# Kernel optimization log

Measured on AMD Instinct MI355X. Metric: run time of the kernel, lower is better.

The kernel has to match this reference:

```python
import jax, jax.numpy as jnp
import numpy as np

B, S, D = 32, 512, 512
GH, LH = 8, 4            # global / local num_heads
W, STRIDE = 10, 5        # local window size and hop (window_size // 2)


def _mha(x, w_in, b_in, w_out, b_out, n_heads, key_mask=None):
    """Torch nn.MultiheadAttention (self-attn, eval mode). x: [N, L, D]."""
    N, L, d = x.shape
    dh = d // n_heads
    qkv = x @ w_in.T + b_in                       # [N, L, 3D]
    q, k, v = jnp.split(qkv, 3, axis=-1)
    def heads(t):
        return t.reshape(N, L, n_heads, dh).transpose(0, 2, 1, 3)  # [N,H,L,dh]
    q, k, v = heads(q), heads(k), heads(v)
    scores = jnp.einsum('bhqd,bhkd->bhqk', q, k) / jnp.sqrt(jnp.asarray(dh, x.dtype))
    if key_mask is not None:                      # key_mask: [N, L] bool, True = valid
        scores = jnp.where(key_mask[:, None, None, :], scores, jnp.asarray(-1e9, x.dtype))
    attn = jax.nn.softmax(scores, axis=-1)
    out = jnp.einsum('bhqk,bhkd->bhqd', attn, v).transpose(0, 2, 1, 3).reshape(N, L, d)
    return out @ w_out.T + b_out


def setup_inputs() -> dict:
    key = jax.random.key(0)
    ks = jax.random.split(key, 12)
    s = 0.02
    return {
        'x':      jax.random.normal(ks[0], (B, S, D), jnp.float32),
        'gw_in':  jax.random.normal(ks[1], (3 * D, D), jnp.float32) * s,
        'gb_in':  jnp.zeros((3 * D,), jnp.float32),
        'gw_out': jax.random.normal(ks[2], (D, D), jnp.float32) * s,
        'gb_out': jnp.zeros((D,), jnp.float32),
        'lw_in':  jax.random.normal(ks[3], (3 * D, D), jnp.float32) * s,
        'lb_in':  jnp.zeros((3 * D,), jnp.float32),
        'lw_out': jax.random.normal(ks[4], (D, D), jnp.float32) * s,
        'lb_out': jnp.zeros((D,), jnp.float32),
        'fw':     jax.random.normal(ks[5], (D, 2 * D), jnp.float32) * s,
        'fb':     jnp.zeros((D,), jnp.float32),
    }


def reference(x, gw_in, gb_in, gw_out, gb_out, lw_in, lb_in, lw_out, lb_out, fw, fb):
    # ---- global branch: full self-attention over the sequence ----
    global_out = _mha(x, gw_in, gb_in, gw_out, gb_out, GH)

    # ---- local branch: overlapping windows of size W, hop STRIDE ----
    starts = np.arange(0, S, STRIDE)              # static window starts
    NW = len(starts)
    pos = starts[:, None] + np.arange(W)          # [NW, W] absolute positions
    valid = pos < S                               # ragged tail windows
    idx = np.minimum(pos, S - 1)                  # clipped gather indices

    windows = x[:, idx]                           # [B, NW, W, D]
    windows = windows.reshape(B * NW, W, D)
    key_mask = jnp.broadcast_to(jnp.asarray(valid)[None], (B, NW, W)).reshape(B * NW, W)

    local_attn = _mha(windows, lw_in, lb_in, lw_out, lb_out, LH, key_mask=key_mask)
    local_attn = local_attn.reshape(B, NW, W, D) * jnp.asarray(valid)[None, :, :, None].astype(x.dtype)

    # scatter-add overlapping window outputs back (matches `local_out[:, i:end] +=`)
    local_out = jnp.zeros_like(x).at[:, idx.reshape(-1)].add(local_attn.reshape(B, NW * W, D))

    # ---- fusion MLP (dropout = identity in eval) ----
    combined = jnp.concatenate([global_out, local_out], axis=-1)   # [B, S, 2D]
    return jax.nn.relu(combined @ fw.T + fb)
```

## Files before the change

kernel.cpp:

```cpp
#include <hip/hip_runtime.h>
#include <cstdint>
#include <cstddef>

#define DEV __device__ __forceinline__

typedef float f32x4 __attribute__((ext_vector_type(4)));
typedef short bf16x8 __attribute__((ext_vector_type(8)));

DEV unsigned short f2bf(float f) {
  union { float f; unsigned u; } v; v.f = f;
  unsigned u = v.u;
  unsigned r = u + 0x7FFFu + ((u >> 16) & 1u);
  return (unsigned short)(r >> 16);
}
DEV unsigned short f2bf_hu(float f) {
  union { float f; unsigned u; } v; v.f = f;
  return (unsigned short)((v.u + 0x8000u) >> 16);
}
DEV float bf2f(unsigned short h) {
  union { unsigned u; float f; } v; v.u = ((unsigned)h) << 16;
  return v.f;
}

DEV void gload16(const void* g, void* l) {
  __builtin_amdgcn_global_load_lds((const __attribute__((address_space(1))) unsigned int*)g,
                                   (__attribute__((address_space(3))) unsigned int*)l,
                                   16, 0, 0);
}

DEV f32x4 MFMA(bf16x8 a, bf16x8 b, f32x4 c) {
  return __builtin_amdgcn_mfma_f32_16x16x32_bf16(a, b, c, 0, 0, 0);
}

__global__ void k_f2bf(const float* __restrict__ src, unsigned short* __restrict__ dst, int n) {
  int i = (blockIdx.x * blockDim.x + threadIdx.x) * 4;
  int stride = gridDim.x * blockDim.x * 4;
  for (; i < n; i += stride) {
    float4 v = *(const float4*)(src + i);
    ushort4 o;
    o.x = f2bf(v.x); o.y = f2bf(v.y); o.z = f2bf(v.z); o.w = f2bf(v.w);
    *(ushort4*)(dst + i) = o;
  }
}

__global__ __launch_bounds__(256) void k_merge(const float* __restrict__ fw,
                                               const float* __restrict__ gw_out,
                                               const float* __restrict__ lw_out,
                                               unsigned short* __restrict__ M1b,
                                               unsigned short* __restrict__ M2b) {
  __shared__ float Fa[64][68];
  __shared__ float Gb[64][68];
  const int bi = blockIdx.x, bj = blockIdx.y, m2 = blockIdx.z;
  const float* g = m2 ? lw_out : gw_out;
  const int i0 = bi * 64, j0 = bj * 64;
  const int tid = threadIdx.x;
  const int tr = tid >> 4, tc = tid & 15;
  float acc[4][4] = {};
  for (int kc = 0; kc < 8; kc++) {
    int k0 = kc * 64;
    __syncthreads();
    #pragma unroll
    for (int it = 0; it < 4; it++) {
      int r = tr + 16 * it;
      float4 v = *(const float4*)(fw + (size_t)(i0 + r) * 1024 + m2 * 512 + k0 + tc * 4);
      Fa[tc * 4 + 0][r] = v.x; Fa[tc * 4 + 1][r] = v.y;
      Fa[tc * 4 + 2][r] = v.z; Fa[tc * 4 + 3][r] = v.w;
      *(float4*)&Gb[r][tc * 4] = *(const float4*)(g + (size_t)(k0 + r) * 512 + j0 + tc * 4);
    }
    __syncthreads();
    for (int k = 0; k < 64; k++) {
      float4 a4 = *(const float4*)&Fa[k][tr * 4];
      float4 b4 = *(const float4*)&Gb[k][tc * 4];
      float av[4] = {a4.x, a4.y, a4.z, a4.w};
      float bv[4] = {b4.x, b4.y, b4.z, b4.w};
      #pragma unroll
      for (int r = 0; r < 4; r++)
        #pragma unroll
        for (int c = 0; c < 4; c++)
          acc[r][c] += av[r] * bv[c];
    }
  }
  unsigned short* M = m2 ? M2b : M1b;
  #pragma unroll
  for (int r = 0; r < 4; r++) {
    ushort4 pk;
    pk.x = f2bf(acc[r][0]); pk.y = f2bf(acc[r][1]);
    pk.z = f2bf(acc[r][2]); pk.w = f2bf(acc[r][3]);
    *(ushort4*)&M[(size_t)(i0 + tr * 4 + r) * 512 + j0 + tc * 4] = pk;
  }
}

__global__ __launch_bounds__(256) void k_bias(const float* __restrict__ fw, const float* __restrict__ gb_out,
                                              const float* __restrict__ lb_out, const float* __restrict__ fb,
                                              float* __restrict__ bias1, float* __restrict__ bias2) {
  __shared__ float bv[512];
  const int which = blockIdx.y;
  const int i0 = blockIdx.x * 64;
  const float* src = which ? lb_out : gb_out;
  for (int t = threadIdx.x; t < 512; t += 256) bv[t] = src[t];
  __syncthreads();
  const int r = threadIdx.x >> 2, c4 = threadIdx.x & 3;
  const float* frow = fw + (size_t)(i0 + r) * 1024 + (which ? 512 : 0) + c4 * 128;
  float a = 0.f;
  #pragma unroll 4
  for (int k = 0; k < 128; k += 4) {
    float4 v = *(const float4*)(frow + k);
    a += v.x * bv[c4 * 128 + k] + v.y * bv[c4 * 128 + k + 1]
       + v.z * bv[c4 * 128 + k + 2] + v.w * bv[c4 * 128 + k + 3];
  }
  a += __shfl_xor(a, 1);
  a += __shfl_xor(a, 2);
  if (c4 == 0) {
    int i = i0 + r;
    if (which) bias2[i] = a;
    else       bias1[i] = a + fb[i];
  }
}

template <int EPI>
__global__ __launch_bounds__(256) void k_gemm(const unsigned short* __restrict__ A,
                                              const unsigned short* __restrict__ A2,
                                              const unsigned short* __restrict__ Wm,
                                              const unsigned short* __restrict__ W2,
                                              const float* __restrict__ bias,
                                              const float* __restrict__ bias2,
                                              float qscale, void* __restrict__ Cout,
                                              int Ntot, int NT) {
  __shared__ unsigned short As[2][128 * 32];
  __shared__ unsigned short Bs[2][128 * 32];
  const int tid = threadIdx.x;
  const int wave = tid >> 6, lane = tid & 63;
  const int wr = wave >> 1, wc = wave & 1;
  const int bm = blockIdx.x, bn = blockIdx.y;
  const int ql = lane & 15, kg = lane >> 4;

  const int c0 = wave * 2;
  const int srow = lane >> 2;
  const int sks = (lane & 3) * 8;

  auto stage = [&](int buf, int t) {
    const unsigned short* sA = A;
    const unsigned short* sW = Wm;
    int k0 = t * 32;
    if (EPI == 1 && t >= 16) { sA = A2; sW = W2; k0 = (t - 16) * 32; }
    #pragma unroll
    for (int i = 0; i < 2; i++) {
      int c = c0 + i;
      int row = c * 16 + srow;
      gload16(sA + (size_t)(bm * 128 + row) * 512 + k0 + sks, &As[buf][c * 512 + lane * 8]);
      gload16(sW + (size_t)(bn * 128 + row) * 512 + k0 + sks, &Bs[buf][c * 512 + lane * 8]);
    }
  };

  f32x4 acc[4][4] = {};
  stage(0, 0);
  __syncthreads();
  for (int t = 0; t < NT; t++) {
    int buf = t & 1;
    if (t + 1 < NT) stage(buf ^ 1, t + 1);
    const unsigned short* as = As[buf];
    const unsigned short* bs = Bs[buf];
    bf16x8 af[4], bfr[4];
    #pragma unroll
    for (int m = 0; m < 4; m++)
      af[m] = *(const bf16x8*)&as[(wr * 64 + m * 16 + ql) * 32 + kg * 8];
    #pragma unroll
    for (int n = 0; n < 4; n++)
      bfr[n] = *(const bf16x8*)&bs[(wc * 64 + n * 16 + ql) * 32 + kg * 8];
    #pragma unroll
    for (int m = 0; m < 4; m++)
      #pragma unroll
      for (int n = 0; n < 4; n++)
        acc[m][n] = MFMA(af[m], bfr[n], acc[m][n]);
    __syncthreads();
  }

  const int row0 = bm * 128 + wr * 64;
  const int col0 = bn * 128 + wc * 64;
  if (EPI == 0) {
    unsigned short* C = (unsigned short*)Cout;
    #pragma unroll
    for (int m = 0; m < 4; m++)
      #pragma unroll
      for (int n = 0; n < 4; n++) {
        int col = col0 + n * 16 + ql;
        float bcol = bias[col];
        float qs = (col < 512) ? qscale : 1.0f;
        #pragma unroll
        for (int r = 0; r < 4; r++) {
          int row = row0 + m * 16 + kg * 4 + r;
          C[(size_t)row * Ntot + col] = f2bf((acc[m][n][r] + bcol) * qs);
        }
      }
  } else {
    float* C = (float*)Cout;
    #pragma unroll
    for (int m = 0; m < 4; m++)
      #pragma unroll
      for (int n = 0; n < 4; n++) {
        int col = col0 + n * 16 + ql;
        float b1 = bias[col], b2 = bias2[col];
        #pragma unroll
        for (int r = 0; r < 4; r++) {
          int row = row0 + m * 16 + kg * 4 + r;
          float cc = ((row & 511) < 5) ? 1.0f : 2.0f;
          float v = acc[m][n][r] + b1 + cc * b2;
          C[(size_t)row * 512 + col] = fmaxf(v, 0.0f);
        }
      }
  }
}

__global__ __launch_bounds__(512, 2) void k_attn_g(const unsigned short* __restrict__ QKV,
                                                   unsigned short* __restrict__ Og) {
  __shared__ unsigned short Klds[512 * 64];
  __shared__ unsigned short Vt[64][536];
  __shared__ unsigned short Plds[8][16 * 72];
  const int tid = threadIdx.x, wave = tid >> 6, lane = tid & 63;
  const int ql = lane & 15, kg = lane >> 4;
  const int h = blockIdx.x, b = blockIdx.y;
  const size_t tb = (size_t)b * 512;
  const size_t hoff = (size_t)h * 64;

  #pragma unroll
  for (int i = 0; i < 8; i++) {
    int instr = wave * 8 + i;
    int row = instr * 8 + (lane >> 3);
    int slot = lane & 7;
    int c = slot ^ (row & 7);
    gload16(QKV + (tb + row) * 1536 + 512 + hoff + c * 8, &Klds[instr * 512 + lane * 8]);
  }
  {
    const unsigned short* Vp = QKV + (tb + tid) * 1536 + 1024 + hoff;
    #pragma unroll
    for (int c8 = 0; c8 < 8; c8++) {
      bf16x8 v8 = *(const bf16x8*)(Vp + c8 * 8);
      #pragma unroll
      for (int j = 0; j < 8; j++) Vt[c8 * 8 + j][tid] = (unsigned short)v8[j];
    }
  }
  bf16x8 qf[4][2];
  #pragma unroll
  for (int m = 0; m < 4; m++) {
    const unsigned short* Qp = QKV + (tb + wave * 64 + m * 16 + ql) * 1536 + hoff;
    qf[m][0] = *(const bf16x8*)(Qp + kg * 8);
    qf[m][1] = *(const bf16x8*)(Qp + 32 + kg * 8);
  }
  __syncthreads();

  float l_part[4][4] = {};
  f32x4 o[4][4] = {};
  unsigned short* P = &Plds[wave][0];

  for (int kv = 0; kv < 8; kv++) {
    const int k0 = kv * 64;
    bf16x8 kf[4][2], vb[4][2];
    #pragma unroll
    for (int f = 0; f < 4; f++) {
      int row = k0 + 16 * f + ql;
      #pragma unroll
      for (int c = 0; c < 2; c++)
        kf[f][c] = *(const bf16x8*)&Klds[row * 64 + (((c * 4 + kg) ^ (row & 7)) * 8)];
      #pragma unroll
      for (int st = 0; st < 2; st++)
        vb[f][st] = *(const bf16x8*)&Vt[16 * f + ql][k0 + st * 32 + kg * 8];
    }
    #pragma unroll
    for (int m = 0; m < 4; m++) {
      f32x4 s[4] = {};
      #pragma unroll
      for (int f = 0; f < 4; f++) {
        s[f] = MFMA(qf[m][0], kf[f][0], s[f]);
        s[f] = MFMA(qf[m][1], kf[f][1], s[f]);
      }
      #pragma unroll
      for (int f = 0; f < 4; f++)
        #pragma unroll
        for (int r = 0; r < 4; r++)
          s[f][r] = exp2f(s[f][r]);
      #pragma unroll
      for (int r = 0; r < 4; r++)
        l_part[m][r] += (s[0][r] + s[1][r]) + (s[2][r] + s[3][r]);
      #pragma unroll
      for (int f = 0; f < 4; f++) {
        int chunk = (2 * f + (ql >> 3)) ^ kg;
        #pragma unroll
        for (int r = 0; r < 4; r++)
          P[(kg * 4 + r) * 72 + chunk * 8 + (ql & 7)] = f2bf_hu(s[f][r]);
      }
      #pragma unroll
      for (int st = 0; st < 2; st++) {
        bf16x8 pa = *(const bf16x8*)&P[ql * 72 + (((st * 4 + kg) ^ (ql >> 2)) * 8)];
        #pragma unroll
        for (int f = 0; f < 4; f++)
          o[m][f] = MFMA(pa, vb[f][st], o[m][f]);
      }
    }
  }

  #pragma unroll
  for (int m = 0; m < 4; m++)
    #pragma unroll
    for (int r = 0; r < 4; r++) {
      float l = l_part[m][r];
      l += __shfl_xor(l, 1);
      l += __shfl_xor(l, 2);
      l += __shfl_xor(l, 4);
      l += __shfl_xor(l, 8);
      float inv = 1.0f / l;
      size_t row = tb + wave * 64 + m * 16 + kg * 4 + r;
      #pragma unroll
      for (int f = 0; f < 4; f++)
        Og[row * 512 + hoff + 16 * f + ql] = f2bf(o[m][f][r] * inv);
    }
}

__global__ __launch_bounds__(256) void k_attn_l(const unsigned short* __restrict__ QKV,
                                                unsigned short* __restrict__ Lacc) {
  __shared__ unsigned short Qs[5][520];
  __shared__ unsigned short Ks[15][520];
  __shared__ unsigned short Vs[15][520];
  __shared__ float Pb[2][4][5][13];
  const int w = blockIdx.x, b = blockIdx.y;
  const int p0 = 5 * w;
  const int tid = threadIdx.x;
  const size_t tbase = (size_t)b * 512;

  for (int c = tid; c < 35 * 64; c += 256) {
    int row = c >> 6, ch = (c & 63) * 8;
    if (row < 5) {
      int tok = min(p0 + row, 511);
      *(bf16x8*)&Qs[row][ch] = *(const bf16x8*)(QKV + (tbase + tok) * 1536 + ch);
    } else if (row < 20) {
      int rr = row - 5;
      int tok = min(max(p0 - 5 + rr, 0), 511);
      *(bf16x8*)&Ks[rr][ch] = *(const bf16x8*)(QKV + (tbase + tok) * 1536 + 512 + ch);
    } else {
      int rr = row - 20;
      int tok = min(max(p0 - 5 + rr, 0), 511);
      *(bf16x8*)&Vs[rr][ch] = *(const bf16x8*)(QKV + (tbase + tok) * 1536 + 1024 + ch);
    }
  }
  __syncthreads();

  #pragma unroll
  for (int rep = 0; rep < 2; rep++) {
    int idx = tid + rep * 256;
    if (idx < 400) {
      int j = idx % 10;
      int t1 = idx / 10;
      int q = t1 % 5;
      int t2 = t1 / 5;
      int h = t2 & 3;
      int win = t2 >> 2;
      int krow = win ? j : j + 5;
      int ktok = p0 - 5 + krow;
      float scv = -1e30f;
      bool ok = (win == 0 || w > 0) && (p0 + q < 512) && (ktok < 512);
      if (ok) {
        float acc = 0.f;
        const unsigned short* qp = &Qs[q][h * 128];
        const unsigned short* kp = &Ks[krow][h * 128];
        #pragma unroll
        for (int ck = 0; ck < 16; ck++) {
          bf16x8 q8 = *(const bf16x8*)(qp + ck * 8);
          bf16x8 k8 = *(const bf16x8*)(kp + ck * 8);
          #pragma unroll
          for (int e = 0; e < 8; e++)
            acc += bf2f((unsigned short)q8[e]) * bf2f((unsigned short)k8[e]);
        }
        scv = acc;
      }
      Pb[win][h][q][j] = scv;
    }
  }
  __syncthreads();

  if (tid < 40) {
    int q = tid % 5;
    int t2 = tid / 5;
    int h = t2 & 3;
    int win = t2 >> 2;
    float* row = &Pb[win][h][q][0];
    float mx = -1e30f;
    #pragma unroll
    for (int j = 0; j < 10; j++) mx = fmaxf(mx, row[j]);
    float e[10]; float su = 0.f;
    #pragma unroll
    for (int j = 0; j < 10; j++) {
      float v = row[j];
      float ej = (v <= -1e29f) ? 0.f : exp2f(v - mx);
      e[j] = ej; su += ej;
    }
    float inv = (su > 0.f) ? 1.0f / su : 0.f;
    #pragma unroll
    for (int j = 0; j < 10; j++) row[j] = e[j] * inv;
  }
  __syncthreads();

  {
    const int h = tid >> 6;
    const int d = tid * 2;
    for (int qq = 0; qq < 5; qq++) {
      int p = p0 + qq;
      if (p >= 512) break;
      float a0 = 0.f, a1 = 0.f;
      const float* P0 = &Pb[0][h][qq][0];
      #pragma unroll
      for (int j = 0; j < 10; j++) {
        float pw = P0[j];
        a0 += pw * bf2f(Vs[j + 5][d]);
        a1 += pw * bf2f(Vs[j + 5][d + 1]);
      }
      if (w > 0) {
        const float* P1 = &Pb[1][h][qq][0];
        #pragma unroll
        for (int j = 0; j < 10; j++) {
          float pw = P1[j];
          a0 += pw * bf2f(Vs[j][d]);
          a1 += pw * bf2f(Vs[j][d + 1]);
        }
      }
      ushort2 st; st.x = f2bf(a0); st.y = f2bf(a1);
      *(ushort2*)&Lacc[(tbase + p) * 512 + d] = st;
    }
  }
}

extern "C" void kernel_launch(void* const* d_in, const int* in_sizes, int n_in,
                              void* d_out, int out_size, void* d_ws, size_t ws_size,
                              hipStream_t stream) {
  const float* x      = (const float*)d_in[0];
  const float* gw_in  = (const float*)d_in[1];
  const float* gb_in  = (const float*)d_in[2];
  const float* gw_out = (const float*)d_in[3];
  const float* gb_out = (const float*)d_in[4];
  const float* lw_in  = (const float*)d_in[5];
  const float* lb_in  = (const float*)d_in[6];
  const float* lw_out = (const float*)d_in[7];
  const float* lb_out = (const float*)d_in[8];
  const float* fw     = (const float*)d_in[9];
  const float* fb     = (const float*)d_in[10];

  char* ws = (char*)d_ws;
  auto alloc = [&](size_t bytes) -> char* {
    char* p = ws;
    ws += (bytes + 255) & ~(size_t)255;
    return p;
  };
  unsigned short* xb     = (unsigned short*)alloc((size_t)16384 * 512 * 2);
  unsigned short* gwin_b = (unsigned short*)alloc((size_t)1536 * 512 * 2);
  unsigned short* lwin_b = (unsigned short*)alloc((size_t)1536 * 512 * 2);
  unsigned short* M1b    = (unsigned short*)alloc((size_t)512 * 512 * 2);
  unsigned short* M2b    = (unsigned short*)alloc((size_t)512 * 512 * 2);
  float* bias1           = (float*)alloc(512 * 4);
  float* bias2           = (float*)alloc(512 * 4);
  unsigned short* QKV    = (unsigned short*)alloc((size_t)16384 * 1536 * 2);
  unsigned short* Og     = (unsigned short*)alloc((size_t)16384 * 512 * 2);
  unsigned short* La     = (unsigned short*)alloc((size_t)16384 * 512 * 2);

  k_f2bf<<<2048, 256, 0, stream>>>(x, xb, 16384 * 512);
  k_f2bf<<<128, 256, 0, stream>>>(gw_in, gwin_b, 1536 * 512);
  k_f2bf<<<128, 256, 0, stream>>>(lw_in, lwin_b, 1536 * 512);
  k_merge<<<dim3(8, 8, 2), 256, 0, stream>>>(fw, gw_out, lw_out, M1b, M2b);
  k_bias<<<dim3(8, 2), 256, 0, stream>>>(fw, gb_out, lb_out, fb, bias1, bias2);

  k_gemm<0><<<dim3(128, 12), 256, 0, stream>>>(xb, nullptr, gwin_b, nullptr, gb_in, nullptr,
                                               0.125f * 1.44269504f, QKV, 1536, 16);
  k_attn_g<<<dim3(8, 32), 512, 0, stream>>>(QKV, Og);

  k_gemm<0><<<dim3(128, 12), 256, 0, stream>>>(xb, nullptr, lwin_b, nullptr, lb_in, nullptr,
                                               0.08838834764831845f * 1.44269504f, QKV, 1536, 16);
  k_attn_l<<<dim3(103, 32), 256, 0, stream>>>(QKV, La);

  k_gemm<1><<<dim3(128, 4), 256, 0, stream>>>(Og, La, M1b, M2b, bias1, bias2,
                                              1.0f, d_out, 512, 32);
}
```

Before: 220.4 us.

## Replace QKV projection GEMM with 256x256-tile pipelined kernel using 8 waves

Adds a new bf16 MFMA GEMM kernel with 256x256 output tiles, 512 threads, and double-buffered LDS staging through global_load_lds. The K=64 step is split into four phases, each with explicit vmcnt waits, barriers and s_setprio around the MFMA bursts, so loads of the next tile overlap compute. Blocks are remapped with a swizzle for L2 locality. The larger tile raises data reuse per block and cuts the grid from 1536 to 384 blocks per projection, at the cost of more registers and LDS and possibly fewer waves in flight.

```diff
diff --git a/kernel.cpp b/kernel.cpp
--- a/kernel.cpp
+++ b/kernel.cpp
@@ -6,6 +6,11 @@
 
 typedef float f32x4 __attribute__((ext_vector_type(4)));
 typedef short bf16x8 __attribute__((ext_vector_type(8)));
+
+#define BARRIER() asm volatile("s_barrier" ::: "memory")
+#define VMCNT0()  asm volatile("s_waitcnt vmcnt(0)" ::: "memory")
+#define VMCNT2()  asm volatile("s_waitcnt vmcnt(2)" ::: "memory")
+#define VMCNT4()  asm volatile("s_waitcnt vmcnt(4)" ::: "memory")
 
 DEV unsigned short f2bf(float f) {
   union { float f; unsigned u; } v; v.f = f;
@@ -115,6 +120,144 @@
     if (which) bias2[i] = a;
     else       bias1[i] = a + fb[i];
   }
+}
+
+__global__ __launch_bounds__(512, 2) void k_gemm256(const unsigned short* __restrict__ A,
+                                                    const unsigned short* __restrict__ Wm,
+                                                    const float* __restrict__ bias,
+                                                    float qscale,
+                                                    unsigned short* __restrict__ Cout,
+                                                    int Ntot, int NBN, int NS) {
+  __shared__ unsigned short As[2][2][8192];
+  __shared__ unsigned short Bs[2][2][8192];
+  const int tid = threadIdx.x, wave = tid >> 6, lane = tid & 63;
+  const int wr = wave >> 2, wc = wave & 3;
+  const int ql = lane & 15, kg = lane >> 4;
+
+  const int cpx = gridDim.x >> 3;
+  const int swz = ((int)blockIdx.x & 7) * cpx + ((int)blockIdx.x >> 3);
+  const int bm = swz / NBN, bn = swz % NBN;
+
+  const int lineoff = (ql >> 1) * 64 + ((((ql & 1) * 4 + kg) ^ ((ql >> 1) & 7)) * 8);
+  const int aoff = wr * 4096 + lineoff;
+  const int boff = wc * 2048 + lineoff;
+
+  auto stage = [&](const unsigned short* __restrict__ src, int grow0, int gcol0,
+                   unsigned short* dst) {
+    #pragma unroll
+    for (int i = 0; i < 2; i++) {
+      int n = tid + i * 512;
+      int p = n >> 3, s = n & 7;
+      int v = s ^ (p & 7);
+      gload16(src + (size_t)(grow0 + p * 2 + (v >> 2)) * 512 + gcol0 + (v & 3) * 8,
+              dst + n * 8);
+    }
+  };
+
+  f32x4 acc[8][4] = {};
+
+  stage(A, bm * 256, 0, As[0][0]);
+  stage(Wm, bn * 256, 0, Bs[0][0]);
+  stage(A, bm * 256, 32, As[0][1]);
+  stage(Wm, bn * 256, 32, Bs[0][1]);
+  VMCNT4();
+  BARRIER();
+
+  for (int T = 0; T < NS; T++) {
+    const int c = T & 1, nc = c ^ 1;
+    const bool pre = (T + 1 < NS);
+    const int g0 = (T + 1) * 64;
+
+    bf16x8 br[4];
+    {
+      const unsigned short* ab = As[c][0] + aoff;
+      const unsigned short* bb = Bs[c][0] + boff;
+      bf16x8 a_[4];
+      #pragma unroll
+      for (int mm = 0; mm < 4; mm++) a_[mm] = *(const bf16x8*)(ab + mm * 512);
+      #pragma unroll
+      for (int nq = 0; nq < 4; nq++) br[nq] = *(const bf16x8*)(bb + nq * 512);
+      if (pre) stage(A, bm * 256, g0, As[nc][0]);
+      BARRIER();
+      __builtin_amdgcn_s_setprio(1);
+      #pragma unroll
+      for (int mm = 0; mm < 4; mm++)
+        #pragma unroll
+        for (int nq = 0; nq < 4; nq++)
+          acc[mm][nq] = MFMA(a_[mm], br[nq], acc[mm][nq]);
+      __builtin_amdgcn_s_setprio(0);
+      BARRIER();
+    }
+    {
+      if (pre) { VMCNT2(); } else { VMCNT0(); }
+      const unsigned short* ab = As[c][0] + aoff + 2048;
+      bf16x8 a_[4];
+      #pragma unroll
+      for (int mm = 0; mm < 4; mm++) a_[mm] = *(const bf16x8*)(ab + mm * 512);
+      if (pre) stage(Wm, bn * 256, g0, Bs[nc][0]);
+      BARRIER();
+      __builtin_amdgcn_s_setprio(1);
+      #pragma unroll
+      for (int mm = 0; mm < 4; mm++)
+        #pragma unroll
+        for (int nq = 0; nq < 4; nq++)
+          acc[4 + mm][nq] = MFMA(a_[mm], br[nq], acc[4 + mm][nq]);
+      __builtin_amdgcn_s_setprio(0);
+      BARRIER();
+    }
+    {
+      const unsigned short* ab = As[c][1] + aoff;
+      const unsigned short* bb = Bs[c][1] + boff;
+      bf16x8 a_[4];
+      #pragma unroll
+      for (int mm = 0; mm < 4; mm++) a_[mm] = *(const bf16x8*)(ab + mm * 512);
+      #pragma unroll
+      for (int nq = 0; nq < 4; nq++) br[nq] = *(const bf16x8*)(bb + nq * 512);
+      if (pre) stage(A, bm * 256, g0 + 32, As[nc][1]);
+      BARRIER();
+      __builtin_amdgcn_s_setprio(1);
+      #pragma unroll
+      for (int mm = 0; mm < 4; mm++)
+        #pragma unroll
+        for (int nq = 0; nq < 4; nq++)
+          acc[mm][nq] = MFMA(a_[mm], br[nq], acc[mm][nq]);
+      __builtin_amdgcn_s_setprio(0);
+      BARRIER();
+    }
+    {
+      VMCNT2();
+      const unsigned short* ab = As[c][1] + aoff + 2048;
+      bf16x8 a_[4];
+      #pragma unroll
+      for (int mm = 0; mm < 4; mm++) a_[mm] = *(const bf16x8*)(ab + mm * 512);
+      if (pre) stage(Wm, bn * 256, g0 + 32, Bs[nc][1]);
+      BARRIER();
+      __builtin_amdgcn_s_setprio(1);
+      #pragma unroll
+      for (int mm = 0; mm < 4; mm++)
+        #pragma unroll
+        for (int nq = 0; nq < 4; nq++)
+          acc[4 + mm][nq] = MFMA(a_[mm], br[nq], acc[4 + mm][nq]);
+      __builtin_amdgcn_s_setprio(0);
+      BARRIER();
+    }
+  }
+
+  const int row0 = bm * 256 + wr * 128;
+  const int col0 = bn * 256 + wc * 64;
+  #pragma unroll
+  for (int mq = 0; mq < 8; mq++)
+    #pragma unroll
+    for (int nq = 0; nq < 4; nq++) {
+      int col = col0 + nq * 16 + ql;
+      float bcol = bias[col];
+      float qs = (col < 512) ? qscale : 1.0f;
+      #pragma unroll
+      for (int r = 0; r < 4; r++) {
+        int row = row0 + mq * 16 + kg * 4 + r;
+        Cout[(size_t)row * Ntot + col] = f2bf((acc[mq][nq][r] + bcol) * qs);
+      }
+    }
 }
 
 template <int EPI>
@@ -465,12 +608,12 @@
   k_merge<<<dim3(8, 8, 2), 256, 0, stream>>>(fw, gw_out, lw_out, M1b, M2b);
   k_bias<<<dim3(8, 2), 256, 0, stream>>>(fw, gb_out, lb_out, fb, bias1, bias2);
 
-  k_gemm<0><<<dim3(128, 12), 256, 0, stream>>>(xb, nullptr, gwin_b, nullptr, gb_in, nullptr,
-                                               0.125f * 1.44269504f, QKV, 1536, 16);
+  k_gemm256<<<dim3(384), 512, 0, stream>>>(xb, gwin_b, gb_in, 0.125f * 1.44269504f,
+                                           QKV, 1536, 6, 8);
   k_attn_g<<<dim3(8, 32), 512, 0, stream>>>(QKV, Og);
 
-  k_gemm<0><<<dim3(128, 12), 256, 0, stream>>>(xb, nullptr, lwin_b, nullptr, lb_in, nullptr,
-                                               0.08838834764831845f * 1.44269504f, QKV, 1536, 16);
+  k_gemm256<<<dim3(384), 512, 0, stream>>>(xb, lwin_b, lb_in, 0.08838834764831845f * 1.44269504f,
+                                           QKV, 1536, 6, 8);
   k_attn_l<<<dim3(103, 32), 256, 0, stream>>>(QKV, La);
 
   k_gemm<1><<<dim3(128, 4), 256, 0, stream>>>(Og, La, M1b, M2b, bias1, bias2,
```

Result: slower. 230.9 us (+4.8%).

## Transpose QK^T MFMA and pack P with cvt_pk_bf16 in global attention

Applied to the files above, without the earlier changes.

The S=QK^T MFMA operands are swapped so each lane holds four consecutive key scores for one query. This lets P be packed two values at a time with v_cvt_pk_bf16_f32 and written as 8-byte stores into an unpadded, XOR-swizzled LDS tile, instead of scalar 2-byte stores. The V-transpose buffer drops its padding in favour of an XOR swizzle, and the row-sum reduction moves to fewer cross-lane shuffles plus a final broadcast shuffle. The aim is to cut LDS store count, bank conflicts and VALU conversion work in the inner loop. In exchange, rounding of P changes from round-half-up to the hardware conversion mode, and the swizzle indexing must stay correct.

```diff
diff --git a/kernel.cpp b/kernel.cpp
--- a/kernel.cpp
+++ b/kernel.cpp
@@ -13,13 +13,14 @@
   unsigned r = u + 0x7FFFu + ((u >> 16) & 1u);
   return (unsigned short)(r >> 16);
 }
-DEV unsigned short f2bf_hu(float f) {
-  union { float f; unsigned u; } v; v.f = f;
-  return (unsigned short)((v.u + 0x8000u) >> 16);
-}
 DEV float bf2f(unsigned short h) {
   union { unsigned u; float f; } v; v.u = ((unsigned)h) << 16;
   return v.f;
+}
+DEV unsigned cvtpk(float lo, float hi) {
+  unsigned r;
+  asm("v_cvt_pk_bf16_f32 %0, %1, %2" : "=v"(r) : "v"(lo), "v"(hi));
+  return r;
 }
 
 DEV void gload16(const void* g, void* l) {
@@ -214,8 +215,8 @@
 __global__ __launch_bounds__(512, 2) void k_attn_g(const unsigned short* __restrict__ QKV,
                                                    unsigned short* __restrict__ Og) {
   __shared__ unsigned short Klds[512 * 64];
-  __shared__ unsigned short Vt[64][536];
-  __shared__ unsigned short Plds[8][16 * 72];
+  __shared__ unsigned short Vt[64 * 512];
+  __shared__ unsigned short Plds[8][16 * 64];
   const int tid = threadIdx.x, wave = tid >> 6, lane = tid & 63;
   const int ql = lane & 15, kg = lane >> 4;
   const int h = blockIdx.x, b = blockIdx.y;
@@ -232,11 +233,15 @@
   }
   {
     const unsigned short* Vp = QKV + (tb + tid) * 1536 + 1024 + hoff;
+    const int kc = tid >> 3, ke = tid & 7;
     #pragma unroll
     for (int c8 = 0; c8 < 8; c8++) {
       bf16x8 v8 = *(const bf16x8*)(Vp + c8 * 8);
       #pragma unroll
-      for (int j = 0; j < 8; j++) Vt[c8 * 8 + j][tid] = (unsigned short)v8[j];
+      for (int j = 0; j < 8; j++) {
+        int d = c8 * 8 + j;
+        Vt[d * 512 + (((kc ^ (d & 7)) << 3) | ke)] = (unsigned short)v8[j];
+      }
     }
   }
   bf16x8 qf[4][2];
@@ -248,9 +253,10 @@
   }
   __syncthreads();
 
-  float l_part[4][4] = {};
+  float l_part[4] = {};
   f32x4 o[4][4] = {};
-  unsigned short* P = &Plds[wave][0];
+  unsigned short* Pw = &Plds[wave][0];
+  const int pswz = 2 * (ql & 7);
 
   for (int kv = 0; kv < 8; kv++) {
     const int k0 = kv * 64;
@@ -262,35 +268,34 @@
       for (int c = 0; c < 2; c++)
         kf[f][c] = *(const bf16x8*)&Klds[row * 64 + (((c * 4 + kg) ^ (row & 7)) * 8)];
       #pragma unroll
-      for (int st = 0; st < 2; st++)
-        vb[f][st] = *(const bf16x8*)&Vt[16 * f + ql][k0 + st * 32 + kg * 8];
+      for (int st = 0; st < 2; st++) {
+        int d = 16 * f + ql;
+        int ch = (k0 >> 3) + st * 4 + kg;
+        vb[f][st] = *(const bf16x8*)&Vt[d * 512 + ((ch ^ (d & 7)) * 8)];
+      }
     }
     #pragma unroll
     for (int m = 0; m < 4; m++) {
       f32x4 s[4] = {};
       #pragma unroll
       for (int f = 0; f < 4; f++) {
-        s[f] = MFMA(qf[m][0], kf[f][0], s[f]);
-        s[f] = MFMA(qf[m][1], kf[f][1], s[f]);
-      }
-      #pragma unroll
-      for (int f = 0; f < 4; f++)
+        s[f] = MFMA(kf[f][0], qf[m][0], s[f]);
+        s[f] = MFMA(kf[f][1], qf[m][1], s[f]);
+      }
+      #pragma unroll
+      for (int f = 0; f < 4; f++) {
         #pragma unroll
         for (int r = 0; r < 4; r++)
           s[f][r] = exp2f(s[f][r]);
-      #pragma unroll
-      for (int r = 0; r < 4; r++)
-        l_part[m][r] += (s[0][r] + s[1][r]) + (s[2][r] + s[3][r]);
-      #pragma unroll
-      for (int f = 0; f < 4; f++) {
-        int chunk = (2 * f + (ql >> 3)) ^ kg;
-        #pragma unroll
-        for (int r = 0; r < 4; r++)
-          P[(kg * 4 + r) * 72 + chunk * 8 + (ql & 7)] = f2bf_hu(s[f][r]);
+        l_part[m] += (s[f][0] + s[f][1]) + (s[f][2] + s[f][3]);
+        uint2 pk;
+        pk.x = cvtpk(s[f][0], s[f][1]);
+        pk.y = cvtpk(s[f][2], s[f][3]);
+        *(uint2*)&Pw[ql * 64 + (((4 * f + kg) ^ pswz) * 4)] = pk;
       }
       #pragma unroll
       for (int st = 0; st < 2; st++) {
-        bf16x8 pa = *(const bf16x8*)&P[ql * 72 + (((st * 4 + kg) ^ (ql >> 2)) * 8)];
+        bf16x8 pa = *(const bf16x8*)&Pw[ql * 64 + (((8 * st + 2 * kg) ^ pswz) * 4)];
         #pragma unroll
         for (int f = 0; f < 4; f++)
           o[m][f] = MFMA(pa, vb[f][st], o[m][f]);
@@ -299,20 +304,19 @@
   }
 
   #pragma unroll
-  for (int m = 0; m < 4; m++)
+  for (int m = 0; m < 4; m++) {
+    float l = l_part[m];
+    l += __shfl_xor(l, 16);
+    l += __shfl_xor(l, 32);
     #pragma unroll
     for (int r = 0; r < 4; r++) {
-      float l = l_part[m][r];
-      l += __shfl_xor(l, 1);
-      l += __shfl_xor(l, 2);
-      l += __shfl_xor(l, 4);
-      l += __shfl_xor(l, 8);
-      float inv = 1.0f / l;
+      float inv = 1.0f / __shfl(l, kg * 4 + r);
       size_t row = tb + wave * 64 + m * 16 + kg * 4 + r;
       #pragma unroll
       for (int f = 0; f < 4; f++)
         Og[row * 512 + hoff + 16 * f + ql] = f2bf(o[m][f][r] * inv);
     }
+  }
 }
 
 __global__ __launch_bounds__(256) void k_attn_l(const unsigned short* __restrict__ QKV,
```

After: 220.9 us. About the same (+0.2%).

## Use 1024-thread blocks in global attention with XOR-swizzled V and P LDS

Applied to the files above, without the earlier changes.

The global attention kernel now runs 16 waves per block, each handling 32 query rows instead of 64. This halves per-wave accumulator registers and spreads K/V staging across more threads. The transposed V and per-wave P buffers move from padded layouts to XOR-swizzled layouts to avoid LDS bank conflicts without padding. LDS use per block grows slightly with the extra P buffers. Each wave now amortises its K/V fragment loads over fewer rows, and the launch bound of 4 blocks per CU is unlikely to be met given the LDS size.

```diff
diff --git a/kernel.cpp b/kernel.cpp
--- a/kernel.cpp
+++ b/kernel.cpp
@@ -211,11 +211,11 @@
   }
 }
 
-__global__ __launch_bounds__(512, 2) void k_attn_g(const unsigned short* __restrict__ QKV,
-                                                   unsigned short* __restrict__ Og) {
+__global__ __launch_bounds__(1024, 4) void k_attn_g(const unsigned short* __restrict__ QKV,
+                                                    unsigned short* __restrict__ Og) {
   __shared__ unsigned short Klds[512 * 64];
-  __shared__ unsigned short Vt[64][536];
-  __shared__ unsigned short Plds[8][16 * 72];
+  __shared__ unsigned short Vt[64 * 512];
+  __shared__ unsigned short Plds[16][16 * 64];
   const int tid = threadIdx.x, wave = tid >> 6, lane = tid & 63;
   const int ql = lane & 15, kg = lane >> 4;
   const int h = blockIdx.x, b = blockIdx.y;
@@ -223,34 +223,40 @@
   const size_t hoff = (size_t)h * 64;
 
   #pragma unroll
-  for (int i = 0; i < 8; i++) {
-    int instr = wave * 8 + i;
+  for (int i = 0; i < 4; i++) {
+    int instr = wave * 4 + i;
     int row = instr * 8 + (lane >> 3);
     int slot = lane & 7;
     int c = slot ^ (row & 7);
     gload16(QKV + (tb + row) * 1536 + 512 + hoff + c * 8, &Klds[instr * 512 + lane * 8]);
   }
   {
-    const unsigned short* Vp = QKV + (tb + tid) * 1536 + 1024 + hoff;
-    #pragma unroll
-    for (int c8 = 0; c8 < 8; c8++) {
-      bf16x8 v8 = *(const bf16x8*)(Vp + c8 * 8);
-      #pragma unroll
-      for (int j = 0; j < 8; j++) Vt[c8 * 8 + j][tid] = (unsigned short)v8[j];
-    }
-  }
-  bf16x8 qf[4][2];
+    int key = tid & 511;
+    int cbase = (tid >> 9) * 4;
+    const unsigned short* Vp = QKV + (tb + key) * 1536 + 1024 + hoff;
+    const int kc = key >> 3, ke = key & 7;
+    #pragma unroll
+    for (int c8 = 0; c8 < 4; c8++) {
+      bf16x8 v8 = *(const bf16x8*)(Vp + (cbase + c8) * 8);
+      #pragma unroll
+      for (int j = 0; j < 8; j++) {
+        int d = (cbase + c8) * 8 + j;
+        Vt[d * 512 + ((kc ^ (d & 7)) * 8 + ke)] = (unsigned short)v8[j];
+      }
+    }
+  }
+  bf16x8 qf[2][2];
   #pragma unroll
-  for (int m = 0; m < 4; m++) {
-    const unsigned short* Qp = QKV + (tb + wave * 64 + m * 16 + ql) * 1536 + hoff;
+  for (int m = 0; m < 2; m++) {
+    const unsigned short* Qp = QKV + (tb + wave * 32 + m * 16 + ql) * 1536 + hoff;
     qf[m][0] = *(const bf16x8*)(Qp + kg * 8);
     qf[m][1] = *(const bf16x8*)(Qp + 32 + kg * 8);
   }
   __syncthreads();
 
-  float l_part[4][4] = {};
-  f32x4 o[4][4] = {};
-  unsigned short* P = &Plds[wave][0];
+  float l_part[2][4] = {};
+  f32x4 o[2][4] = {};
+  unsigned short* Pw = &Plds[wave][0];
 
   for (int kv = 0; kv < 8; kv++) {
     const int k0 = kv * 64;
@@ -262,11 +268,14 @@
       for (int c = 0; c < 2; c++)
         kf[f][c] = *(const bf16x8*)&Klds[row * 64 + (((c * 4 + kg) ^ (row & 7)) * 8)];
       #pragma unroll
-      for (int st = 0; st < 2; st++)
-        vb[f][st] = *(const bf16x8*)&Vt[16 * f + ql][k0 + st * 32 + kg * 8];
-    }
-    #pragma unroll
-    for (int m = 0; m < 4; m++) {
+      for (int st = 0; st < 2; st++) {
+        int d = 16 * f + ql;
+        int ch = (k0 >> 3) + st * 4 + kg;
+        vb[f][st] = *(const bf16x8*)&Vt[d * 512 + ((ch ^ (d & 7)) * 8)];
+      }
+    }
+    #pragma unroll
+    for (int m = 0; m < 2; m++) {
       f32x4 s[4] = {};
       #pragma unroll
       for (int f = 0; f < 4; f++) {
@@ -283,14 +292,18 @@
         l_part[m][r] += (s[0][r] + s[1][r]) + (s[2][r] + s[3][r]);
       #pragma unroll
       for (int f = 0; f < 4; f++) {
-        int chunk = (2 * f + (ql >> 3)) ^ kg;
-        #pragma unroll
-        for (int r = 0; r < 4; r++)
-          P[(kg * 4 + r) * 72 + chunk * 8 + (ql & 7)] = f2bf_hu(s[f][r]);
+        int cl = 2 * f + (ql >> 3);
+        #pragma unroll
+        for (int r = 0; r < 4; r++) {
+          int qp = kg * 4 + r;
+          int pos = cl ^ (qp & 7) ^ ((qp >> 3) << 2);
+          Pw[qp * 64 + pos * 8 + (ql & 7)] = f2bf_hu(s[f][r]);
+        }
       }
       #pragma unroll
       for (int st = 0; st < 2; st++) {
-        bf16x8 pa = *(const bf16x8*)&P[ql * 72 + (((st * 4 + kg) ^ (ql >> 2)) * 8)];
+        int pos = (st * 4 + kg) ^ (ql & 7) ^ ((ql >> 3) << 2);
+        bf16x8 pa = *(const bf16x8*)&Pw[ql * 64 + pos * 8];
         #pragma unroll
         for (int f = 0; f < 4; f++)
           o[m][f] = MFMA(pa, vb[f][st], o[m][f]);
@@ -299,7 +312,7 @@
   }
 
   #pragma unroll
-  for (int m = 0; m < 4; m++)
+  for (int m = 0; m < 2; m++)
     #pragma unroll
     for (int r = 0; r < 4; r++) {
       float l = l_part[m][r];
@@ -308,7 +321,7 @@
       l += __shfl_xor(l, 4);
       l += __shfl_xor(l, 8);
       float inv = 1.0f / l;
-      size_t row = tb + wave * 64 + m * 16 + kg * 4 + r;
+      size_t row = tb + wave * 32 + m * 16 + kg * 4 + r;
       #pragma unroll
       for (int f = 0; f < 4; f++)
         Og[row * 512 + hoff + 16 * f + ql] = f2bf(o[m][f][r] * inv);
@@ -467,7 +480,7 @@
 
   k_gemm<0><<<dim3(128, 12), 256, 0, stream>>>(xb, nullptr, gwin_b, nullptr, gb_in, nullptr,
                                                0.125f * 1.44269504f, QKV, 1536, 16);
-  k_attn_g<<<dim3(8, 32), 512, 0, stream>>>(QKV, Og);
+  k_attn_g<<<dim3(8, 32), 1024, 0, stream>>>(QKV, Og);
 
   k_gemm<0><<<dim3(128, 12), 256, 0, stream>>>(xb, nullptr, lwin_b, nullptr, lb_in, nullptr,
                                                0.08838834764831845f * 1.44269504f, QKV, 1536, 16);
```

Result: slower. 225.3 us (+2.2%).
